# Optimization experiments

Measured on AMD Instinct MI355X. Metric: run time of the kernel, lower is better.

The kernel has to match this reference:

```python
import jax, jax.numpy as jnp
import numpy as np

B, T, C = 2, 2048, 1024
NH = 16
HD = C // NH

def setup_inputs() -> dict:
    key = jax.random.key(0)
    k1, k2, k3 = jax.random.split(key, 3)
    x = jax.random.normal(k1, (B, T, C), dtype=jnp.float32)
    w_attn = jax.random.normal(k2, (C, 3 * C), dtype=jnp.float32) * 0.02
    w_proj = jax.random.normal(k3, (C, C), dtype=jnp.float32) * 0.02
    return {"x": x, "w_attn": w_attn, "w_proj": w_proj}

def reference(x, w_attn, w_proj):
    b, t, c = x.shape
    qkv = x @ w_attn                                  # [B,T,3C]
    q, k, v = jnp.split(qkv, 3, axis=-1)
    # [B,NH,T,HD]
    q = q.reshape(b, t, NH, HD).transpose(0, 2, 1, 3)
    k = k.reshape(b, t, NH, HD).transpose(0, 2, 1, 3)
    v = v.reshape(b, t, NH, HD).transpose(0, 2, 1, 3)
    scale = 1.0 / np.sqrt(HD).astype(np.float32)
    att = jnp.einsum('bhqd,bhkd->bhqk', q, k) * scale  # [B,NH,T,T]
    causal = jnp.tril(jnp.ones((t, t), dtype=bool))
    att = jnp.where(causal[None, None], att, jnp.float32(-jnp.inf))
    att = jax.nn.softmax(att, axis=-1)
    y = jnp.einsum('bhqk,bhkd->bhqd', att, v)          # [B,NH,T,HD]
    y = y.transpose(0, 2, 1, 3).reshape(b, t, c)
    return y @ w_proj
```

## Files before the change

### kernel.cpp

```cpp
#include <hip/hip_runtime.h>
#include <hip/hip_bf16.h>

#define BB 2
#define TT 2048
#define CCH 1024
#define NHH 16
#define HDD 64
#define M_TOK (BB*TT)
#define N_QKV (3*CCH)

typedef __attribute__((ext_vector_type(8))) short bf16x8;
typedef __attribute__((ext_vector_type(4))) float f32x4;
typedef unsigned short u16;
typedef unsigned int u32;

__device__ __forceinline__ u16 f2bf(float f) {
    union { float f; u32 u; } v; v.f = f;
    u32 u = v.u;
    u32 r = (u + 0x7FFFu + ((u >> 16) & 1u)) >> 16;
    return (u16)r;
}

__device__ __forceinline__ u32 pk_bf16(float a, float b) {
    u32 ua = __float_as_uint(a) + 0x8000u;
    u32 ub = __float_as_uint(b) + 0x8000u;
    return __builtin_amdgcn_perm(ub, ua, 0x07060302u);
}

__device__ __forceinline__ void async_copy16(const void* g, void* l) {
    __builtin_amdgcn_global_load_lds((__attribute__((address_space(1))) void*)g,
                                     (__attribute__((address_space(3))) void*)l,
                                     16, 0, 0);
}


__global__ __launch_bounds__(256) void cast_bf16_kernel(
    const float* __restrict__ src, u16* __restrict__ dst, int n4) {
    int i = blockIdx.x * 256 + threadIdx.x;
    if (i < n4) {
        float4 f = ((const float4*)src)[i];
        ushort4 o;
        o.x = f2bf(f.x); o.y = f2bf(f.y); o.z = f2bf(f.z); o.w = f2bf(f.w);
        ((ushort4*)dst)[i] = o;
    }
}

__global__ __launch_bounds__(256) void transpose_bf16_kernel(
    const float* __restrict__ src, u16* __restrict__ dst, int R, int Cn,
    int scale_rows, float sc) {
    __shared__ float tile[32][33];
    int c0 = blockIdx.x * 32, r0 = blockIdx.y * 32;
    int tx = threadIdx.x, ty = threadIdx.y;
#pragma unroll
    for (int i = ty; i < 32; i += 8)
        tile[i][tx] = src[(size_t)(r0 + i) * Cn + c0 + tx];
    __syncthreads();
#pragma unroll
    for (int i = ty; i < 32; i += 8) {
        float v = tile[tx][i];
        if (c0 + i < scale_rows) v *= sc;
        dst[(size_t)(c0 + i) * R + r0 + tx] = f2bf(v);
    }
}


#define QKV_NK 16
#define QKV_AS_HALF 16384
#define QKV_BS_HALF 12288
#define QKV_SMEM_BYTES ((2*QKV_AS_HALF + 2*QKV_BS_HALF) * 2)

__global__ __launch_bounds__(512, 1) void qkv_gemm_kernel(
    const u16* __restrict__ A, const u16* __restrict__ Bt,
    u16* __restrict__ Qo, u16* __restrict__ Ko, u16* __restrict__ Vto)
{
    extern __shared__ __align__(16) u16 smem[];
    u16* AsB = smem;
    u16* BsB = smem + 2 * QKV_AS_HALF;
    int t = threadIdx.x;
    int lane = t & 63, w = t >> 6;
    int m0 = blockIdx.y * 256, n0 = blockIdx.x * 192;
    int mw = (w >> 1) * 64, nw = (w & 1) * 96;
    int mr = lane & 15, quad = lane >> 4, swm = mr & 7;

    f32x4 zero = {0.f, 0.f, 0.f, 0.f};
    f32x4 acc[4][6];
#pragma unroll
    for (int i = 0; i < 4; ++i)
#pragma unroll
        for (int j = 0; j < 6; ++j) acc[i][j] = zero;

    int lr = lane >> 3;
    int cswz = (lane & 7) ^ lr;
    const u16* gA[4]; int lAo[4];
#pragma unroll
    for (int p = 0; p < 4; ++p) {
        int grp = w * 4 + p;
        gA[p] = A + (size_t)(m0 + grp * 8 + lr) * CCH + cswz * 8;
        lAo[p] = (grp * 64 + lane) * 8;
    }
    const u16* gB[3]; int lBo[3];
#pragma unroll
    for (int p = 0; p < 3; ++p) {
        int grp = w * 3 + p;
        gB[p] = Bt + (size_t)(n0 + grp * 8 + lr) * CCH + cswz * 8;
        lBo[p] = (grp * 64 + lane) * 8;
    }

#define QKV_STAGE(K0, BUF) do {                                               \
    u16* dA_ = AsB + (BUF) * QKV_AS_HALF;                                     \
    u16* dB_ = BsB + (BUF) * QKV_BS_HALF;                                     \
    _Pragma("unroll") for (int p_ = 0; p_ < 4; ++p_)                          \
        async_copy16(gA[p_] + (K0), dA_ + lAo[p_]);                           \
    _Pragma("unroll") for (int p_ = 0; p_ < 3; ++p_)                          \
        async_copy16(gB[p_] + (K0), dB_ + lBo[p_]);                           \
  } while (0)

    QKV_STAGE(0, 0);
    QKV_STAGE(64, 1);

    for (int k = 0; k < QKV_NK; ++k) {
        int cur = k & 1;
        if (k == QKV_NK - 1) asm volatile("s_waitcnt vmcnt(0)" ::: "memory");
        else                 asm volatile("s_waitcnt vmcnt(7)" ::: "memory");
        __builtin_amdgcn_s_barrier();
        asm volatile("" ::: "memory");
        const u16* Ac = AsB + cur * QKV_AS_HALF;
        const u16* Bc = BsB + cur * QKV_BS_HALF;
        bf16x8 a0[4], a1[4], b0[6], b1[6];
#pragma unroll
        for (int i = 0; i < 4; ++i) {
            int r = (mw + i * 16 + mr) * 64;
            a0[i] = *(const bf16x8*)&Ac[r + ((quad ^ swm) << 3)];
            a1[i] = *(const bf16x8*)&Ac[r + (((quad + 4) ^ swm) << 3)];
        }
#pragma unroll
        for (int j = 0; j < 6; ++j) {
            int r = (nw + j * 16 + mr) * 64;
            b0[j] = *(const bf16x8*)&Bc[r + ((quad ^ swm) << 3)];
            b1[j] = *(const bf16x8*)&Bc[r + (((quad + 4) ^ swm) << 3)];
        }
#pragma unroll
        for (int i = 0; i < 4; ++i)
#pragma unroll
            for (int j = 0; j < 6; ++j)
                acc[i][j] = __builtin_amdgcn_mfma_f32_16x16x32_bf16(b0[j], a0[i], acc[i][j], 0, 0, 0);
        asm volatile("s_waitcnt lgkmcnt(0)" ::: "memory");
        __builtin_amdgcn_sched_barrier(0);
        __builtin_amdgcn_s_barrier();
        asm volatile("" ::: "memory");
        if (k < QKV_NK - 2) QKV_STAGE((k + 2) * 64, cur);
#pragma unroll
        for (int i = 0; i < 4; ++i)
#pragma unroll
            for (int j = 0; j < 6; ++j)
                acc[i][j] = __builtin_amdgcn_mfma_f32_16x16x32_bf16(b1[j], a1[i], acc[i][j], 0, 0, 0);
    }
#undef QKV_STAGE

#pragma unroll
    for (int i = 0; i < 4; ++i)
#pragma unroll
        for (int j = 0; j < 6; ++j) {
            int tok = m0 + mw + i * 16 + mr;
            int cg0 = n0 + nw + j * 16 + quad * 4;
            int part = cg0 >> 10;
            int cc = cg0 & 1023;
            int h = cc >> 6, d0 = cc & 63;
            int b = tok >> 11, tt = tok & 2047;
            int bh = b * NHH + h;
            if (part < 2) {
                u16* dstp = part ? Ko : Qo;
                uint2 o;
                o.x = pk_bf16(acc[i][j][0], acc[i][j][1]);
                o.y = pk_bf16(acc[i][j][2], acc[i][j][3]);
                *(uint2*)&dstp[((size_t)bh * TT + tt) * HDD + d0] = o;
            } else {
#pragma unroll
                for (int r = 0; r < 4; ++r)
                    Vto[((size_t)bh * HDD + d0 + r) * TT + tt] = f2bf(acc[i][j][r]);
            }
        }
}


#define PRJ_NK 16
#define PRJ_AS_HALF 8192
#define PRJ_SMEM_BYTES (4 * PRJ_AS_HALF * 2)

__global__ __launch_bounds__(512, 1) void proj_gemm_kernel(
    const u16* __restrict__ A, const u16* __restrict__ Bt, float* __restrict__ Cout)
{
    extern __shared__ __align__(16) u16 psmem[];
    u16* AsB = psmem;
    u16* BsB = psmem + 2 * PRJ_AS_HALF;
    int t = threadIdx.x;
    int lane = t & 63, w = t >> 6;
    int m0 = blockIdx.y * 128, n0 = blockIdx.x * 128;
    int mw = (w >> 1) * 32, nw = (w & 1) * 64;
    int mr = lane & 15, quad = lane >> 4, swm = mr & 7;

    f32x4 zero = {0.f, 0.f, 0.f, 0.f};
    f32x4 acc[2][4];
#pragma unroll
    for (int i = 0; i < 2; ++i)
#pragma unroll
        for (int j = 0; j < 4; ++j) acc[i][j] = zero;

    int lr = lane >> 3;
    int cswz = (lane & 7) ^ lr;
    const u16* gA[2]; int lAo[2];
#pragma unroll
    for (int p = 0; p < 2; ++p) {
        int grp = w * 2 + p;
        gA[p] = A + (size_t)(m0 + grp * 8 + lr) * CCH + cswz * 8;
        lAo[p] = (grp * 64 + lane) * 8;
    }
    const u16* gB[2]; int lBo[2];
#pragma unroll
    for (int p = 0; p < 2; ++p) {
        int grp = w * 2 + p;
        gB[p] = Bt + (size_t)(n0 + grp * 8 + lr) * CCH + cswz * 8;
        lBo[p] = (grp * 64 + lane) * 8;
    }

#define PRJ_STAGE(K0, BUF) do {                                               \
    u16* dA_ = AsB + (BUF) * PRJ_AS_HALF;                                     \
    u16* dB_ = BsB + (BUF) * PRJ_AS_HALF;                                     \
    _Pragma("unroll") for (int p_ = 0; p_ < 2; ++p_)                          \
        async_copy16(gA[p_] + (K0), dA_ + lAo[p_]);                           \
    _Pragma("unroll") for (int p_ = 0; p_ < 2; ++p_)                          \
        async_copy16(gB[p_] + (K0), dB_ + lBo[p_]);                           \
  } while (0)

    PRJ_STAGE(0, 0);
    PRJ_STAGE(64, 1);

    for (int k = 0; k < PRJ_NK; ++k) {
        int cur = k & 1;
        if (k == PRJ_NK - 1) asm volatile("s_waitcnt vmcnt(0)" ::: "memory");
        else                 asm volatile("s_waitcnt vmcnt(4)" ::: "memory");
        __builtin_amdgcn_s_barrier();
        asm volatile("" ::: "memory");
        const u16* Ac = AsB + cur * PRJ_AS_HALF;
        const u16* Bc = BsB + cur * PRJ_AS_HALF;
        bf16x8 a0[2], a1[2], b0[4], b1[4];
#pragma unroll
        for (int i = 0; i < 2; ++i) {
            int r = (mw + i * 16 + mr) * 64;
            a0[i] = *(const bf16x8*)&Ac[r + ((quad ^ swm) << 3)];
            a1[i] = *(const bf16x8*)&Ac[r + (((quad + 4) ^ swm) << 3)];
        }
#pragma unroll
        for (int j = 0; j < 4; ++j) {
            int r = (nw + j * 16 + mr) * 64;
            b0[j] = *(const bf16x8*)&Bc[r + ((quad ^ swm) << 3)];
            b1[j] = *(const bf16x8*)&Bc[r + (((quad + 4) ^ swm) << 3)];
        }
#pragma unroll
        for (int i = 0; i < 2; ++i)
#pragma unroll
            for (int j = 0; j < 4; ++j)
                acc[i][j] = __builtin_amdgcn_mfma_f32_16x16x32_bf16(b0[j], a0[i], acc[i][j], 0, 0, 0);
        asm volatile("s_waitcnt lgkmcnt(0)" ::: "memory");
        __builtin_amdgcn_sched_barrier(0);
        __builtin_amdgcn_s_barrier();
        asm volatile("" ::: "memory");
        if (k < PRJ_NK - 2) PRJ_STAGE((k + 2) * 64, cur);
#pragma unroll
        for (int i = 0; i < 2; ++i)
#pragma unroll
            for (int j = 0; j < 4; ++j)
                acc[i][j] = __builtin_amdgcn_mfma_f32_16x16x32_bf16(b1[j], a1[i], acc[i][j], 0, 0, 0);
    }
#undef PRJ_STAGE

#pragma unroll
    for (int i = 0; i < 2; ++i)
#pragma unroll
        for (int j = 0; j < 4; ++j) {
            int tok = m0 + mw + i * 16 + mr;
            int cg0 = n0 + nw + j * 16 + quad * 4;
            float4 v;
            v.x = acc[i][j][0]; v.y = acc[i][j][1];
            v.z = acc[i][j][2]; v.w = acc[i][j][3];
            *(float4*)&Cout[(size_t)tok * CCH + cg0] = v;
        }
}


#define PST2 40

template<bool MASK>
__device__ __forceinline__ void tile3(
    const u16* __restrict__ Kb, const u16* __restrict__ Vb, u16* __restrict__ pb,
    bf16x8 qf0, bf16x8 qf1, bf16x8 ones, int m, int quad, int sw, int kh,
    int kvb, int qcol, f32x4 (&o)[4], f32x4& lacc)
{
    f32x4 zero = {0.f, 0.f, 0.f, 0.f};
#pragma unroll
    for (int kc = 0; kc < 2; ++kc) {
        int rr = kh * 32 + kc * 16 + m;
        bf16x8 kf0 = *(const bf16x8*)&Kb[rr * 64 + ((quad ^ sw) << 3)];
        bf16x8 kf1 = *(const bf16x8*)&Kb[rr * 64 + (((quad + 4) ^ sw) << 3)];
        f32x4 s  = __builtin_amdgcn_mfma_f32_16x16x32_bf16(kf0, qf0, zero, 0, 0, 0);
        f32x4 st = __builtin_amdgcn_mfma_f32_16x16x32_bf16(kf1, qf1, s, 0, 0, 0);
        float e0, e1, e2, e3;
#pragma unroll
        for (int r = 0; r < 4; ++r) {
            float v = st[r];
            if (MASK && (kvb + kc * 16 + quad * 4 + r > qcol)) v = -1e30f;
            float e = __builtin_amdgcn_exp2f(v);
            if (r == 0) e0 = e; else if (r == 1) e1 = e; else if (r == 2) e2 = e; else e3 = e;
        }
        uint2 pk; pk.x = pk_bf16(e0, e1); pk.y = pk_bf16(e2, e3);
        *(uint2*)&pb[m * PST2 + kc * 16 + quad * 4] = pk;
    }
    bf16x8 pf = *(const bf16x8*)&pb[m * PST2 + quad * 8];
    lacc = __builtin_amdgcn_mfma_f32_16x16x32_bf16(ones, pf, lacc, 0, 0, 0);
#pragma unroll
    for (int dg = 0; dg < 4; ++dg) {
        int rr = dg * 16 + m;
        bf16x8 vf = *(const bf16x8*)&Vb[rr * 64 + (((kh * 4 + quad) ^ sw) << 3)];
        o[dg] = __builtin_amdgcn_mfma_f32_16x16x32_bf16(vf, pf, o[dg], 0, 0, 0);
    }
}

#define ATTN_SM_U16 35072
#define ATTN_SMEM_BYTES (ATTN_SM_U16 * 2)

__global__ __launch_bounds__(512, 2) void attn_kernel(
    const u16* __restrict__ Q, const u16* __restrict__ K,
    const u16* __restrict__ Vt, u16* __restrict__ Y)
{
    extern __shared__ __align__(16) u16 asmem[];
    int t = threadIdx.x;
    int w = t >> 6, lane = t & 63;
    int m = lane & 15, quad = lane >> 4;
    int iq = w >> 1, kh = w & 1;

    int bid = blockIdx.x;
    int head = bid & 31;
    int g = bid >> 5;
    int pr = (g < 8) ? g : 23 - g;
    int qbA = pr;
    int qbB = 31 - pr;
    int rbA = qbA * 64 + iq * 16;
    int rbB = qbB * 64 + iq * 16;

    const u16* qpA = Q + ((size_t)head * TT + rbA + m) * HDD + quad * 8;
    const u16* qpB = Q + ((size_t)head * TT + rbB + m) * HDD + quad * 8;
    bf16x8 qA0 = *(const bf16x8*)qpA;
    bf16x8 qA1 = *(const bf16x8*)(qpA + 32);
    bf16x8 qB0 = *(const bf16x8*)qpB;
    bf16x8 qB1 = *(const bf16x8*)(qpB + 32);

    bf16x8 ones;
#pragma unroll
    for (int i = 0; i < 8; ++i) ones[i] = (short)0x3F80;

    const u16* kbase = K + (size_t)head * TT * HDD;
    const u16* vbase = Vt + (size_t)head * HDD * TT;
    u16* pbA = asmem + 24576 + (w * 2 + 0) * (16 * PST2);
    u16* pbB = asmem + 24576 + (w * 2 + 1) * (16 * PST2);

    int lr = lane >> 3;
    int cg = (lane & 7) ^ lr;
    int r0 = w * 8 + lr;
    int loff = (w * 64 + lane) * 8;

    f32x4 zero = {0.f, 0.f, 0.f, 0.f};
    f32x4 oA[4], oB[4], laA = zero, laB = zero;
#pragma unroll
    for (int dg = 0; dg < 4; ++dg) { oA[dg] = zero; oB[dg] = zero; }
    int qcA = rbA + m, qcB = rbB + m;
    int sw = m & 7;

    const u16* kst = kbase + (size_t)r0 * 64 + cg * 8;
    const u16* vst = vbase + (size_t)r0 * TT + cg * 8;

    async_copy16(kst, asmem + loff);
    async_copy16(vst, asmem + 12288 + loff);
    kst += 64 * HDD; vst += 64;
    async_copy16(kst, asmem + 4096 + loff);
    async_copy16(vst, asmem + 16384 + loff);
    kst += 64 * HDD; vst += 64;

#define ATTN_CHUNK(KBUF, VBUF, IC) do {                                             \
    int kvb_ = ((IC) << 6) + kh * 32;                                               \
    if ((IC) < qbA)                                                                 \
        tile3<false>(KBUF, VBUF, pbA, qA0, qA1, ones, m, quad, sw, kh, kvb_, qcA, oA, laA); \
    else if ((IC) == qbA)                                                           \
        tile3<true >(KBUF, VBUF, pbA, qA0, qA1, ones, m, quad, sw, kh, kvb_, qcA, oA, laA); \
    if ((IC) < qbB)                                                                 \
        tile3<false>(KBUF, VBUF, pbB, qB0, qB1, ones, m, quad, sw, kh, kvb_, qcB, oB, laB); \
    else                                                                            \
        tile3<true >(KBUF, VBUF, pbB, qB0, qB1, ones, m, quad, sw, kh, kvb_, qcB, oB, laB); \
  } while (0)

#define ATTN_BODY(IC, KBUF, VBUF, PKBUF, PVBUF) do {                                \
    if ((IC) < qbB) asm volatile("s_waitcnt vmcnt(2) lgkmcnt(0)" ::: "memory");     \
    else            asm volatile("s_waitcnt vmcnt(0) lgkmcnt(0)" ::: "memory");     \
    __builtin_amdgcn_s_barrier();                                                   \
    asm volatile("" ::: "memory");                                                  \
    if ((IC) + 2 <= qbB) {                                                          \
        async_copy16(kst, (PKBUF) + loff);                                          \
        async_copy16(vst, (PVBUF) + loff);                                          \
        kst += 64 * HDD; vst += 64;                                                 \
    }                                                                               \
    ATTN_CHUNK(KBUF, VBUF, IC);                                                     \
  } while (0)

    int ic = 0;
    while (ic + 2 <= qbB) {
        ATTN_BODY(ic,     asmem,        asmem + 12288, asmem + 8192, asmem + 20480);
        ATTN_BODY(ic + 1, asmem + 4096, asmem + 16384, asmem,        asmem + 12288);
        ATTN_BODY(ic + 2, asmem + 8192, asmem + 20480, asmem + 4096, asmem + 16384);
        ic += 3;
    }
    if (ic <= qbB) {
        ATTN_BODY(ic, asmem, asmem + 12288, asmem + 8192, asmem + 20480);
        ++ic;
    }
    if (ic <= qbB) {
        ATTN_BODY(ic, asmem + 4096, asmem + 16384, asmem, asmem + 12288);
        ++ic;
    }
#undef ATTN_BODY
#undef ATTN_CHUNK

    float lA = laA[0];
    float lB = laB[0];

    __syncthreads();
    f32x4* ob = (f32x4*)asmem;
    float* lb = (float*)&asmem[34816];
    if (kh) {
        f32x4* dst = ob + (size_t)iq * 512 + lane;
#pragma unroll
        for (int dg = 0; dg < 4; ++dg) {
            dst[dg * 64] = oA[dg];
            dst[(4 + dg) * 64] = oB[dg];
        }
        if (quad == 0) {
            lb[(iq * 2 + 0) * 16 + m] = lA;
            lb[(iq * 2 + 1) * 16 + m] = lB;
        }
    }
    __syncthreads();
    if (!kh) {
        f32x4* src = ob + (size_t)iq * 512 + lane;
#pragma unroll
        for (int dg = 0; dg < 4; ++dg) {
            oA[dg] += src[dg * 64];
            oB[dg] += src[(4 + dg) * 64];
        }
        lA += lb[(iq * 2 + 0) * 16 + m];
        lB += lb[(iq * 2 + 1) * 16 + m];
        float invA = 1.0f / lA, invB = 1.0f / lB;

        int b = head >> 4, h = head & 15;
        size_t roA = ((size_t)(b * TT + rbA + m)) * CCH + h * HDD;
        size_t roB = ((size_t)(b * TT + rbB + m)) * CCH + h * HDD;
#pragma unroll
        for (int dg = 0; dg < 4; ++dg) {
            uint2 ov;
            ov.x = pk_bf16(oA[dg][0] * invA, oA[dg][1] * invA);
            ov.y = pk_bf16(oA[dg][2] * invA, oA[dg][3] * invA);
            *(uint2*)&Y[roA + dg * 16 + quad * 4] = ov;
            ov.x = pk_bf16(oB[dg][0] * invB, oB[dg][1] * invB);
            ov.y = pk_bf16(oB[dg][2] * invB, oB[dg][3] * invB);
            *(uint2*)&Y[roB + dg * 16 + quad * 4] = ov;
        }
    }
}


extern "C" void kernel_launch(void* const* d_in, const int* in_sizes, int n_in,
                              void* d_out, int out_size, void* d_ws, size_t ws_size,
                              hipStream_t stream) {
    const float* x      = (const float*)d_in[0];
    const float* w_attn = (const float*)d_in[1];
    const float* w_proj = (const float*)d_in[2];
    float* out = (float*)d_out;

    char* ws = (char*)d_ws;
    u16* x_bf   = (u16*)ws; ws += (size_t)M_TOK * CCH * 2;
    u16* wqkvT  = (u16*)ws; ws += (size_t)N_QKV * CCH * 2;
    u16* wprojT = (u16*)ws; ws += (size_t)CCH * CCH * 2;
    u16* qbuf   = (u16*)ws; ws += (size_t)BB * NHH * TT * HDD * 2;
    u16* kbuf   = (u16*)ws; ws += (size_t)BB * NHH * TT * HDD * 2;
    u16* vtb    = (u16*)ws; ws += (size_t)BB * NHH * HDD * TT * 2;
    u16* yb     = (u16*)ws; ws += (size_t)M_TOK * CCH * 2;

    static bool attr_done = false;
    if (!attr_done) {
        (void)hipFuncSetAttribute(reinterpret_cast<const void*>(qkv_gemm_kernel),
                                  hipFuncAttributeMaxDynamicSharedMemorySize,
                                  QKV_SMEM_BYTES);
        (void)hipFuncSetAttribute(reinterpret_cast<const void*>(proj_gemm_kernel),
                                  hipFuncAttributeMaxDynamicSharedMemorySize,
                                  PRJ_SMEM_BYTES);
        (void)hipFuncSetAttribute(reinterpret_cast<const void*>(attn_kernel),
                                  hipFuncAttributeMaxDynamicSharedMemorySize,
                                  ATTN_SMEM_BYTES);
        attr_done = true;
    }

    const float QSC = 0.125f * 1.44269504088896f;

    cast_bf16_kernel<<<dim3(M_TOK * CCH / 4 / 256), dim3(256), 0, stream>>>(x, x_bf, M_TOK * CCH / 4);
    transpose_bf16_kernel<<<dim3(N_QKV / 32, CCH / 32), dim3(32, 8), 0, stream>>>(
        w_attn, wqkvT, CCH, N_QKV, CCH, QSC);
    transpose_bf16_kernel<<<dim3(CCH / 32, CCH / 32), dim3(32, 8), 0, stream>>>(
        w_proj, wprojT, CCH, CCH, 0, 1.0f);
    qkv_gemm_kernel<<<dim3(16, 16), dim3(512), QKV_SMEM_BYTES, stream>>>(
        x_bf, wqkvT, qbuf, kbuf, vtb);
    attn_kernel<<<dim3(512), dim3(512), ATTN_SMEM_BYTES, stream>>>(qbuf, kbuf, vtb, yb);
    proj_gemm_kernel<<<dim3(8, 32), dim3(512), PRJ_SMEM_BYTES, stream>>>(
        yb, wprojT, out);
}
```

Before: 166.7 us.

## Process one contiguous 128-row query block per workgroup, sharing K/V fragments

Each attention workgroup used to handle two 64-row query blocks taken from opposite ends of the sequence. It now handles a single 128-row query block, where each warp owns two adjacent 16-row sub-tiles. K and V fragments are read from shared memory once per chunk and reused for both sub-tiles, and the QK and PV phases are interleaved to hide latency. The cost is that workgroups no longer have equal causal work: lighter and heavier blocks now differ in how many KV chunks they process, which can leave the grid with a long tail.

```diff
diff --git a/kernel.cpp b/kernel.cpp
--- a/kernel.cpp
+++ b/kernel.cpp
@@ -291,19 +291,16 @@
 #define PST2 40
 
 template<bool MASK>
-__device__ __forceinline__ void tile3(
-    const u16* __restrict__ Kb, const u16* __restrict__ Vb, u16* __restrict__ pb,
-    bf16x8 qf0, bf16x8 qf1, bf16x8 ones, int m, int quad, int sw, int kh,
-    int kvb, int qcol, f32x4 (&o)[4], f32x4& lacc)
+__device__ __forceinline__ void tile_qk2(
+    const bf16x8 (&kf)[2][2], u16* __restrict__ pb,
+    bf16x8 qf0, bf16x8 qf1, int m, int quad,
+    int kvb, int qcol)
 {
     f32x4 zero = {0.f, 0.f, 0.f, 0.f};
 #pragma unroll
     for (int kc = 0; kc < 2; ++kc) {
-        int rr = kh * 32 + kc * 16 + m;
-        bf16x8 kf0 = *(const bf16x8*)&Kb[rr * 64 + ((quad ^ sw) << 3)];
-        bf16x8 kf1 = *(const bf16x8*)&Kb[rr * 64 + (((quad + 4) ^ sw) << 3)];
-        f32x4 s  = __builtin_amdgcn_mfma_f32_16x16x32_bf16(kf0, qf0, zero, 0, 0, 0);
-        f32x4 st = __builtin_amdgcn_mfma_f32_16x16x32_bf16(kf1, qf1, s, 0, 0, 0);
+        f32x4 s  = __builtin_amdgcn_mfma_f32_16x16x32_bf16(kf[kc][0], qf0, zero, 0, 0, 0);
+        f32x4 st = __builtin_amdgcn_mfma_f32_16x16x32_bf16(kf[kc][1], qf1, s, 0, 0, 0);
         float e0, e1, e2, e3;
 #pragma unroll
         for (int r = 0; r < 4; ++r) {
@@ -315,14 +312,20 @@
         uint2 pk; pk.x = pk_bf16(e0, e1); pk.y = pk_bf16(e2, e3);
         *(uint2*)&pb[m * PST2 + kc * 16 + quad * 4] = pk;
     }
-    bf16x8 pf = *(const bf16x8*)&pb[m * PST2 + quad * 8];
+}
+
+__device__ __forceinline__ bf16x8 load_pf(const u16* __restrict__ pb, int m, int quad) {
+    return *(const bf16x8*)&pb[m * PST2 + quad * 8];
+}
+
+__device__ __forceinline__ void tile_pv2(
+    const bf16x8 (&vf)[4], bf16x8 pf, bf16x8 ones,
+    f32x4 (&o)[4], f32x4& lacc)
+{
     lacc = __builtin_amdgcn_mfma_f32_16x16x32_bf16(ones, pf, lacc, 0, 0, 0);
 #pragma unroll
-    for (int dg = 0; dg < 4; ++dg) {
-        int rr = dg * 16 + m;
-        bf16x8 vf = *(const bf16x8*)&Vb[rr * 64 + (((kh * 4 + quad) ^ sw) << 3)];
-        o[dg] = __builtin_amdgcn_mfma_f32_16x16x32_bf16(vf, pf, o[dg], 0, 0, 0);
-    }
+    for (int dg = 0; dg < 4; ++dg)
+        o[dg] = __builtin_amdgcn_mfma_f32_16x16x32_bf16(vf[dg], pf, o[dg], 0, 0, 0);
 }
 
 #define ATTN_SM_U16 35072
@@ -341,18 +344,16 @@
     int bid = blockIdx.x;
     int head = bid & 31;
     int g = bid >> 5;
-    int pr = (g < 8) ? g : 23 - g;
-    int qbA = pr;
-    int qbB = 31 - pr;
-    int rbA = qbA * 64 + iq * 16;
-    int rbB = qbB * 64 + iq * 16;
-
-    const u16* qpA = Q + ((size_t)head * TT + rbA + m) * HDD + quad * 8;
-    const u16* qpB = Q + ((size_t)head * TT + rbB + m) * HDD + quad * 8;
-    bf16x8 qA0 = *(const bf16x8*)qpA;
-    bf16x8 qA1 = *(const bf16x8*)(qpA + 32);
-    bf16x8 qB0 = *(const bf16x8*)qpB;
-    bf16x8 qB1 = *(const bf16x8*)(qpB + 32);
+    int qb = (g < 8) ? g : 23 - g;
+    int lim = 2 * qb + 1;
+    int rb = qb * 128 + iq * 32;
+
+    const u16* qp0 = Q + ((size_t)head * TT + rb + m) * HDD + quad * 8;
+    const u16* qp1 = Q + ((size_t)head * TT + rb + 16 + m) * HDD + quad * 8;
+    bf16x8 q00 = *(const bf16x8*)qp0;
+    bf16x8 q01 = *(const bf16x8*)(qp0 + 32);
+    bf16x8 q10 = *(const bf16x8*)qp1;
+    bf16x8 q11 = *(const bf16x8*)(qp1 + 32);
 
     bf16x8 ones;
 #pragma unroll
@@ -360,8 +361,8 @@
 
     const u16* kbase = K + (size_t)head * TT * HDD;
     const u16* vbase = Vt + (size_t)head * HDD * TT;
-    u16* pbA = asmem + 24576 + (w * 2 + 0) * (16 * PST2);
-    u16* pbB = asmem + 24576 + (w * 2 + 1) * (16 * PST2);
+    u16* pb0 = asmem + 24576 + (w * 2 + 0) * (16 * PST2);
+    u16* pb1 = asmem + 24576 + (w * 2 + 1) * (16 * PST2);
 
     int lr = lane >> 3;
     int cg = (lane & 7) ^ lr;
@@ -369,10 +370,10 @@
     int loff = (w * 64 + lane) * 8;
 
     f32x4 zero = {0.f, 0.f, 0.f, 0.f};
-    f32x4 oA[4], oB[4], laA = zero, laB = zero;
-#pragma unroll
-    for (int dg = 0; dg < 4; ++dg) { oA[dg] = zero; oB[dg] = zero; }
-    int qcA = rbA + m, qcB = rbB + m;
+    f32x4 o0[4], o1[4], la0 = zero, la1 = zero;
+#pragma unroll
+    for (int dg = 0; dg < 4; ++dg) { o0[dg] = zero; o1[dg] = zero; }
+    int qc0 = rb + m, qc1 = rb + 16 + m;
     int sw = m & 7;
 
     const u16* kst = kbase + (size_t)r0 * 64 + cg * 8;
@@ -387,22 +388,33 @@
 
 #define ATTN_CHUNK(KBUF, VBUF, IC) do {                                             \
     int kvb_ = ((IC) << 6) + kh * 32;                                               \
-    if ((IC) < qbA)                                                                 \
-        tile3<false>(KBUF, VBUF, pbA, qA0, qA1, ones, m, quad, sw, kh, kvb_, qcA, oA, laA); \
-    else if ((IC) == qbA)                                                           \
-        tile3<true >(KBUF, VBUF, pbA, qA0, qA1, ones, m, quad, sw, kh, kvb_, qcA, oA, laA); \
-    if ((IC) < qbB)                                                                 \
-        tile3<false>(KBUF, VBUF, pbB, qB0, qB1, ones, m, quad, sw, kh, kvb_, qcB, oB, laB); \
-    else                                                                            \
-        tile3<true >(KBUF, VBUF, pbB, qB0, qB1, ones, m, quad, sw, kh, kvb_, qcB, oB, laB); \
+    bool msk_ = (IC) >= 2 * qb;                                                     \
+    bf16x8 kf_[2][2], vf_[4];                                                       \
+    _Pragma("unroll") for (int kc_ = 0; kc_ < 2; ++kc_) {                           \
+        int rr_ = kh * 32 + kc_ * 16 + m;                                           \
+        kf_[kc_][0] = *(const bf16x8*)&(KBUF)[rr_ * 64 + ((quad ^ sw) << 3)];       \
+        kf_[kc_][1] = *(const bf16x8*)&(KBUF)[rr_ * 64 + (((quad + 4) ^ sw) << 3)]; \
+    }                                                                               \
+    _Pragma("unroll") for (int dg_ = 0; dg_ < 4; ++dg_) {                           \
+        int rr_ = dg_ * 16 + m;                                                     \
+        vf_[dg_] = *(const bf16x8*)&(VBUF)[rr_ * 64 + (((kh * 4 + quad) ^ sw) << 3)]; \
+    }                                                                               \
+    if (msk_) tile_qk2<true >(kf_, pb0, q00, q01, m, quad, kvb_, qc0);              \
+    else      tile_qk2<false>(kf_, pb0, q00, q01, m, quad, kvb_, qc0);              \
+    bf16x8 pf0_ = load_pf(pb0, m, quad);                                            \
+    if (msk_) tile_qk2<true >(kf_, pb1, q10, q11, m, quad, kvb_, qc1);              \
+    else      tile_qk2<false>(kf_, pb1, q10, q11, m, quad, kvb_, qc1);              \
+    tile_pv2(vf_, pf0_, ones, o0, la0);                                             \
+    bf16x8 pf1_ = load_pf(pb1, m, quad);                                            \
+    tile_pv2(vf_, pf1_, ones, o1, la1);                                             \
   } while (0)
 
 #define ATTN_BODY(IC, KBUF, VBUF, PKBUF, PVBUF) do {                                \
-    if ((IC) < qbB) asm volatile("s_waitcnt vmcnt(2) lgkmcnt(0)" ::: "memory");     \
+    if ((IC) < lim) asm volatile("s_waitcnt vmcnt(2) lgkmcnt(0)" ::: "memory");     \
     else            asm volatile("s_waitcnt vmcnt(0) lgkmcnt(0)" ::: "memory");     \
     __builtin_amdgcn_s_barrier();                                                   \
     asm volatile("" ::: "memory");                                                  \
-    if ((IC) + 2 <= qbB) {                                                          \
+    if ((IC) + 2 <= lim) {                                                          \
         async_copy16(kst, (PKBUF) + loff);                                          \
         async_copy16(vst, (PVBUF) + loff);                                          \
         kst += 64 * HDD; vst += 64;                                                 \
@@ -411,25 +423,25 @@
   } while (0)
 
     int ic = 0;
-    while (ic + 2 <= qbB) {
+    while (ic + 2 <= lim) {
         ATTN_BODY(ic,     asmem,        asmem + 12288, asmem + 8192, asmem + 20480);
         ATTN_BODY(ic + 1, asmem + 4096, asmem + 16384, asmem,        asmem + 12288);
         ATTN_BODY(ic + 2, asmem + 8192, asmem + 20480, asmem + 4096, asmem + 16384);
         ic += 3;
     }
-    if (ic <= qbB) {
+    if (ic <= lim) {
         ATTN_BODY(ic, asmem, asmem + 12288, asmem + 8192, asmem + 20480);
         ++ic;
     }
-    if (ic <= qbB) {
+    if (ic <= lim) {
         ATTN_BODY(ic, asmem + 4096, asmem + 16384, asmem, asmem + 12288);
         ++ic;
     }
 #undef ATTN_BODY
 #undef ATTN_CHUNK
 
-    float lA = laA[0];
-    float lB = laB[0];
+    float l0 = la0[0];
+    float l1 = la1[0];
 
     __syncthreads();
     f32x4* ob = (f32x4*)asmem;
@@ -438,12 +450,12 @@
         f32x4* dst = ob + (size_t)iq * 512 + lane;
 #pragma unroll
         for (int dg = 0; dg < 4; ++dg) {
-            dst[dg * 64] = oA[dg];
-            dst[(4 + dg) * 64] = oB[dg];
+            dst[dg * 64] = o0[dg];
+            dst[(4 + dg) * 64] = o1[dg];
         }
         if (quad == 0) {
-            lb[(iq * 2 + 0) * 16 + m] = lA;
-            lb[(iq * 2 + 1) * 16 + m] = lB;
+            lb[(iq * 2 + 0) * 16 + m] = l0;
+            lb[(iq * 2 + 1) * 16 + m] = l1;
         }
     }
     __syncthreads();
@@ -451,25 +463,25 @@
         f32x4* src = ob + (size_t)iq * 512 + lane;
 #pragma unroll
         for (int dg = 0; dg < 4; ++dg) {
-            oA[dg] += src[dg * 64];
-            oB[dg] += src[(4 + dg) * 64];
-        }
-        lA += lb[(iq * 2 + 0) * 16 + m];
-        lB += lb[(iq * 2 + 1) * 16 + m];
-        float invA = 1.0f / lA, invB = 1.0f / lB;
+            o0[dg] += src[dg * 64];
+            o1[dg] += src[(4 + dg) * 64];
+        }
+        l0 += lb[(iq * 2 + 0) * 16 + m];
+        l1 += lb[(iq * 2 + 1) * 16 + m];
+        float inv0 = 1.0f / l0, inv1 = 1.0f / l1;
 
         int b = head >> 4, h = head & 15;
-        size_t roA = ((size_t)(b * TT + rbA + m)) * CCH + h * HDD;
-        size_t roB = ((size_t)(b * TT + rbB + m)) * CCH + h * HDD;
+        size_t ro0 = ((size_t)(b * TT + rb + m)) * CCH + h * HDD;
+        size_t ro1 = ((size_t)(b * TT + rb + 16 + m)) * CCH + h * HDD;
 #pragma unroll
         for (int dg = 0; dg < 4; ++dg) {
             uint2 ov;
-            ov.x = pk_bf16(oA[dg][0] * invA, oA[dg][1] * invA);
-            ov.y = pk_bf16(oA[dg][2] * invA, oA[dg][3] * invA);
-            *(uint2*)&Y[roA + dg * 16 + quad * 4] = ov;
-            ov.x = pk_bf16(oB[dg][0] * invB, oB[dg][1] * invB);
-            ov.y = pk_bf16(oB[dg][2] * invB, oB[dg][3] * invB);
-            *(uint2*)&Y[roB + dg * 16 + quad * 4] = ov;
+            ov.x = pk_bf16(o0[dg][0] * inv0, o0[dg][1] * inv0);
+            ov.y = pk_bf16(o0[dg][2] * inv0, o0[dg][3] * inv0);
+            *(uint2*)&Y[ro0 + dg * 16 + quad * 4] = ov;
+            ov.x = pk_bf16(o1[dg][0] * inv1, o1[dg][1] * inv1);
+            ov.y = pk_bf16(o1[dg][2] * inv1, o1[dg][3] * inv1);
+            *(uint2*)&Y[ro1 + dg * 16 + quad * 4] = ov;
         }
     }
 }
```

Result: faster. 161.4 us (-3.2%).
